# Performance work log

Measured on AMD Instinct MI355X. Metric: run time of the kernel, lower is better.

Reference implementation:

```python
import jax, jax.numpy as jnp
import numpy as np

B, K, D, H = 4, 2048, 1024, 16
NCTX = K // 2
IMAGE_SIZE = 224
MAX_POS = 1024


def _build_rope_cache_2d(max_pos, dim, base=10000.0):
    half_dim = dim // 2
    theta = 1.0 / base ** (np.arange(0, half_dim, 2, dtype=np.float32) / half_dim)
    positions = np.arange(max_pos, dtype=np.float32)
    freqs = np.outer(positions, theta)  # [max_pos, dim/4]
    return jnp.asarray(np.stack([np.cos(freqs), np.sin(freqs)], axis=-1))  # [max_pos, dim/4, 2]


def apply_rope_2d(x, coords, rope_cache, image_size):
    b, k, d = x.shape
    half, quarter = d // 2, d // 4
    max_pos = rope_cache.shape[0]
    cn = jnp.clip(coords / image_size * (max_pos - 1), 0, max_pos - 1)
    y_pos = cn[..., 0].astype(jnp.int32)
    x_pos = cn[..., 1].astype(jnp.int32)
    y_rope = rope_cache[y_pos]  # [b,k,quarter,2]
    x_rope = rope_cache[x_pos]

    def rot(part, r):
        c, s = r[..., 0], r[..., 1]
        p0, p1 = part[..., 0], part[..., 1]
        return jnp.stack([p0 * c - p1 * s, p0 * s + p1 * c], -1).reshape(b, k, half)

    xp = x[..., :half].reshape(b, k, quarter, 2)
    yp = x[..., half:].reshape(b, k, quarter, 2)
    return jnp.concatenate([rot(xp, x_rope), rot(yp, y_rope)], -1)


def mha(q_tok, kv_tok, in_w, in_b, out_w, out_b, num_heads):
    b, nq, d = q_tok.shape
    hd = d // num_heads
    wq, wk, wv = jnp.split(in_w, 3, axis=0)
    bq, bk, bv = jnp.split(in_b, 3)
    q = (q_tok @ wq.T + bq).reshape(b, nq, num_heads, hd)
    k = (kv_tok @ wk.T + bk).reshape(b, -1, num_heads, hd)
    v = (kv_tok @ wv.T + bv).reshape(b, -1, num_heads, hd)
    s = jnp.einsum('bqhd,bkhd->bhqk', q, k) / jnp.sqrt(jnp.asarray(hd, q.dtype))
    a = jax.nn.softmax(s, axis=-1)
    o = jnp.einsum('bhqk,bkhd->bqhd', a, v).reshape(b, nq, d)
    return o @ out_w.T + out_b


def setup_inputs() -> dict:
    key = jax.random.key(0)
    ks = jax.random.split(key, 12)
    sc = 1.0 / np.sqrt(D)
    x = jax.random.normal(ks[0], (B, K, D), jnp.float32)
    coords = jax.random.uniform(ks[1], (B, K, 2), jnp.float32) * IMAGE_SIZE
    # boolean context mask with exactly NCTX context tokens per batch (code assumes equal counts)
    perms = jax.vmap(lambda k_: jax.random.permutation(k_, K))(jax.random.split(ks[2], B))
    is_context = jax.vmap(lambda m, i: m.at[i].set(True))(jnp.zeros((B, K), bool), perms[:, :NCTX])
    rope_cache = _build_rope_cache_2d(MAX_POS, D)
    return {
        'x': x, 'coords': coords, 'is_context': is_context, 'rope_cache': rope_cache,
        'ctx_in_w': jax.random.normal(ks[3], (3 * D, D), jnp.float32) * sc,
        'ctx_in_b': jnp.zeros((3 * D,), jnp.float32),
        'ctx_out_w': jax.random.normal(ks[4], (D, D), jnp.float32) * sc,
        'ctx_out_b': jnp.zeros((D,), jnp.float32),
        'tgt_in_w': jax.random.normal(ks[5], (3 * D, D), jnp.float32) * sc,
        'tgt_in_b': jnp.zeros((3 * D,), jnp.float32),
        'tgt_out_w': jax.random.normal(ks[6], (D, D), jnp.float32) * sc,
        'tgt_out_b': jnp.zeros((D,), jnp.float32),
    }


def reference(x, coords, is_context, rope_cache,
              ctx_in_w, ctx_in_b, ctx_out_w, ctx_out_b,
              tgt_in_w, tgt_in_b, tgt_out_w, tgt_out_b):
    # 2D RoPE before attention (as in the backbone)
    xr = apply_rope_2d(x, coords, rope_cache, IMAGE_SIZE)
    # stable argsort: context positions (key 0) first, in original order
    order = jnp.argsort(jnp.where(is_context, 0, 1), axis=1, stable=True)
    ctx_idx = order[:, :NCTX]   # [B, NCTX]
    tgt_idx = order[:, NCTX:]   # [B, K-NCTX]
    ctx_tok = jnp.take_along_axis(xr, ctx_idx[..., None], axis=1)
    tgt_tok = jnp.take_along_axis(xr, tgt_idx[..., None], axis=1)
    ctx_out = mha(ctx_tok, ctx_tok, ctx_in_w, ctx_in_b, ctx_out_w, ctx_out_b, H)
    tgt_out = mha(tgt_tok, ctx_tok, tgt_in_w, tgt_in_b, tgt_out_w, tgt_out_b, H)
    out = jnp.zeros_like(x)
    out = jax.vmap(lambda o, i, v: o.at[i].set(v))(out, ctx_idx, ctx_out)
    out = jax.vmap(lambda o, i, v: o.at[i].set(v))(out, tgt_idx, tgt_out)
    return out
```

## Files before the change

kernel.cpp:

```cpp
#include <hip/hip_runtime.h>
#include <math.h>

#define B_    4
#define K_    2048
#define D_    1024
#define H_    16
#define NCTX_ 1024

typedef unsigned short ushort_t;
typedef _Float16 f16;
typedef __attribute__((ext_vector_type(8))) _Float16 f16x8;
typedef __attribute__((ext_vector_type(4))) float f32x4;

union U4 {
  f16 h[4];
  ushort4 u;
};

union P4 {
  f16 h[4];
  ushort4 u;
};

__device__ __forceinline__ void gload16(const void* g, void* l) {
  __builtin_amdgcn_global_load_lds(
      (const __attribute__((address_space(1))) unsigned int*)g,
      (__attribute__((address_space(3))) unsigned int*)l, 16, 0, 0);
}

__global__ __launch_bounds__(256) void partition_kernel(
    const unsigned char* __restrict__ isctx, int* __restrict__ pos,
    int* __restrict__ ipos) {
  const int b = blockIdx.x;
  const int tid = threadIdx.x;
  const int wid = tid >> 6, lane = tid & 63;
  __shared__ int csum[4];
  __shared__ int waveTot[4];
  __shared__ int strideSh;

  int cnt = 0;
  for (int i = 0; i < 32; ++i) cnt += (isctx[tid * 32 + i] != 0);
  for (int off = 32; off; off >>= 1) cnt += __shfl_down(cnt, off, 64);
  if (lane == 0) csum[wid] = cnt;
  __syncthreads();
  if (tid == 0) {
    int t = csum[0] + csum[1] + csum[2] + csum[3];
    strideSh = (t > 2048) ? 1 : ((t > 768) ? 4 : 8);
  }
  __syncthreads();
  const int stride = strideSh;

  const unsigned char* base = isctx + (size_t)b * K_ * stride;
  int f[8];
  int s = 0;
  for (int i = 0; i < 8; ++i) {
    f[i] = base[(size_t)(tid * 8 + i) * stride] != 0;
    s += f[i];
  }
  int inc = s;
  for (int off = 1; off < 64; off <<= 1) {
    int v = __shfl_up(inc, off, 64);
    if (lane >= off) inc += v;
  }
  if (lane == 63) waveTot[wid] = inc;
  __syncthreads();
  int wOff = 0;
  for (int w = 0; w < wid; ++w) wOff += waveTot[w];
  int run = wOff + inc - s;
  for (int i = 0; i < 8; ++i) {
    int k = tid * 8 + i;
    int p;
    if (f[i]) {
      p = run;
      run++;
    } else {
      p = NCTX_ + k - run;
    }
    pos[b * K_ + k] = p;
    ipos[b * K_ + p] = k;
  }
}

__global__ __launch_bounds__(256) void rope_kernel(
    const float* __restrict__ x, const float* __restrict__ coords,
    const float* __restrict__ cache, const int* __restrict__ ipos,
    f16* __restrict__ tok) {
  const int row = blockIdx.x;
  const int b = row >> 11;
  const int r = row & (K_ - 1);
  const int k = ipos[row];
  const int t = threadIdx.x;

  const float cy = coords[(size_t)(b * K_ + k) * 2 + 0];
  const float cx = coords[(size_t)(b * K_ + k) * 2 + 1];
  const int ypos = (int)fminf(fmaxf(cy / 224.0f * 1023.0f, 0.0f), 1023.0f);
  const int xpos = (int)fminf(fmaxf(cx / 224.0f * 1023.0f, 0.0f), 1023.0f);

  const float4 v = ((const float4*)(x + ((size_t)b * K_ + k) * D_))[t];
  const int e = 4 * t;
  const float* crow;
  int coff;
  if (e < 512) {
    crow = cache + (size_t)xpos * 512;
    coff = e;
  } else {
    crow = cache + (size_t)ypos * 512;
    coff = e - 512;
  }
  const float4 cs = *(const float4*)(crow + coff);
  float o[4];
  o[0] = v.x * cs.x - v.y * cs.y;
  o[1] = v.x * cs.y + v.y * cs.x;
  o[2] = v.z * cs.z - v.w * cs.w;
  o[3] = v.z * cs.w + v.w * cs.z;
  U4 h;
#pragma unroll
  for (int i = 0; i < 4; ++i) h.h[i] = (f16)o[i];
  ((ushort4*)(tok + ((size_t)b * K_ + r) * D_))[t] = h.u;
}

__global__ __launch_bounds__(256) void cvt_all(
    const float* __restrict__ ctx_in_w, const float* __restrict__ tgt_in_w,
    const float* __restrict__ ctx_out_w, const float* __restrict__ tgt_out_w,
    f16* __restrict__ dst) {
  const int i4 = blockIdx.x * 256 + threadIdx.x;
  const int f = i4 * 4;
  const float* src;
  if (f < 3145728) src = ctx_in_w + f;
  else if (f < 5242880) src = tgt_in_w + (f - 3145728 + 1048576);
  else if (f < 6291456) src = tgt_in_w + (f - 5242880);
  else if (f < 7340032) src = ctx_out_w + (f - 6291456);
  else src = tgt_out_w + (f - 7340032);
  const float4 v = *(const float4*)src;
  U4 u;
  u.h[0] = (f16)v.x;
  u.h[1] = (f16)v.y;
  u.h[2] = (f16)v.z;
  u.h[3] = (f16)v.w;
  ((ushort4*)dst)[i4] = u.u;
}

#define GEMM_PRE(AP, WP, Kd)                                                  \
  const int rb_ = wave * 8 + (lane >> 3);          \
  const int kk_ = ((lane & 7) ^ (lane >> 3)) * 8;   \
  const f16* gA_ = (AP) + (size_t)rb_ * (Kd) + kk_;                           \
  const f16* gW_ = (WP) + (size_t)rb_ * (Kd) + kk_;                           \
  const int lA_ = wave * 8 * 64 + lane * 8;

#define GEMM_STAGE(k0s, bb)                                                   \
  _Pragma("unroll") for (int j = 0; j < 4; ++j) {                             \
    gload16(gA_ + (size_t)j * 32 * Kd_ + (k0s), &lds[(bb) + j * 2048 + lA_]); \
    gload16(gW_ + (size_t)j * 32 * Kd_ + (k0s),                               \
            &lds[(bb) + 8192 + j * 2048 + lA_]);                              \
  }

#define GEMM_TILE(bb)                                                         \
  _Pragma("unroll") for (int kh = 0; kh < 2; ++kh) {                          \
    f16x8 af[4], wf[4];                                                       \
    _Pragma("unroll") for (int i = 0; i < 4; ++i) {                           \
      const int ca = ((kh * 4 + quad) ^ (m16 & 7)) * 8;                       \
      af[i] = *(const f16x8*)&lds[(bb) + (wm + i * 16 + m16) * 64 + ca];      \
      wf[i] =                                                                 \
          *(const f16x8*)&lds[(bb) + 8192 + (wn + i * 16 + m16) * 64 + ca];   \
    }                                                                         \
    _Pragma("unroll") for (int i = 0; i < 4; ++i)                             \
        _Pragma("unroll") for (int j = 0; j < 4; ++j)                         \
      acc[i][j] = __builtin_amdgcn_mfma_f32_16x16x32_f16(af[i], wf[j],        \
                                                         acc[i][j], 0, 0, 0); \
  }

#define GEMM_CORE(AP, WP, Kd)                                                 \
  f32x4 acc[4][4];                                                            \
  {                                                                           \
    const f32x4 z = {0.f, 0.f, 0.f, 0.f};                                     \
    for (int i = 0; i < 4; ++i)                                               \
      for (int j = 0; j < 4; ++j) acc[i][j] = z;                              \
  }                                                                           \
  const int Kd_ = (Kd);                                                       \
  GEMM_PRE(AP, WP, Kd_)                                                       \
  GEMM_STAGE(0, 0)                                                            \
  for (int t = 0; t < Kd_ / 64; ++t) {                                        \
    const int cb = (t & 1) * 16384;                                           \
    if (t + 1 < Kd_ / 64) {                                                   \
      GEMM_STAGE((t + 1) * 64, ((t + 1) & 1) * 16384)                         \
      asm volatile("s_waitcnt vmcnt(8)" ::: "memory");                        \
    } else {                                                                  \
      asm volatile("s_waitcnt vmcnt(0)" ::: "memory");                        \
    }                                                                         \
    __builtin_amdgcn_s_barrier();                                             \
    asm volatile("" ::: "memory");                                            \
    GEMM_TILE(cb)                                                             \
    asm volatile("" ::: "memory");                                            \
    __builtin_amdgcn_s_barrier();                                             \
  }

__global__ __launch_bounds__(256, 2) void gemm_proj(
    const f16* __restrict__ tok, const f16* __restrict__ wcat,
    const float* __restrict__ ctx_in_b, const float* __restrict__ tgt_in_b,
    f16* __restrict__ qkvc, f16* __restrict__ kvt, f16* __restrict__ qt) {
  __shared__ f16 lds[32768];
  const int tid = threadIdx.x;
  const int wave = tid >> 6, lane = tid & 63;
  const int quad = lane >> 4, m16 = lane & 15;
  const int nb = blockIdx.x, mb = blockIdx.y, b = blockIdx.z;
  const int wm = (wave & 1) << 6, wn = (wave >> 1) << 6;
  const int m0 = mb * 128;
  const bool isQ = nb >= 40;
  const int n0 = isQ ? (nb - 40) * 128 : nb * 128;
  const f16* AP = tok + (size_t)b * K_ * D_ +
                  (isQ ? (size_t)NCTX_ * D_ : (size_t)0) + (size_t)m0 * D_;
  const f16* WP = wcat + (isQ ? (size_t)5242880 : (size_t)0) +
                  (size_t)n0 * D_;

  GEMM_CORE(AP, WP, D_)

#pragma unroll
  for (int j = 0; j < 4; ++j) {
    const int col = n0 + wn + j * 16 + m16;
    float bv;
    f16* dst;
    int ldc, dcol;
    if (isQ) {
      bv = tgt_in_b[col];
      dst = qt + (size_t)b * NCTX_ * D_;
      ldc = D_;
      dcol = col;
    } else if (col < 3072) {
      bv = ctx_in_b[col];
      dst = qkvc + (size_t)b * NCTX_ * 3072;
      ldc = 3072;
      dcol = col;
    } else {
      bv = tgt_in_b[D_ + col - 3072];
      dst = kvt + (size_t)b * NCTX_ * 2048;
      ldc = 2048;
      dcol = col - 3072;
    }
#pragma unroll
    for (int i = 0; i < 4; ++i) {
      const int mr = m0 + wm + i * 16 + quad * 4;
#pragma unroll
      for (int r = 0; r < 4; ++r)
        dst[(size_t)(mr + r) * ldc + dcol] = (f16)(acc[i][j][r] + bv);
    }
  }
}

__global__ __launch_bounds__(256, 2) void gemm_out(
    const f16* __restrict__ Atok, const f16* __restrict__ Wbase,
    const float* __restrict__ bias_ctx, const float* __restrict__ bias_tgt,
    const int* __restrict__ ipos, float* __restrict__ out) {
  __shared__ f16 lds[32768];
  const int tid = threadIdx.x;
  const int wave = tid >> 6, lane = tid & 63;
  const int quad = lane >> 4, m16 = lane & 15;
  const int n0 = blockIdx.x * 128, m0 = blockIdx.y * 128;
  const int b = blockIdx.z & 3, sel = blockIdx.z >> 2;
  const int wm = (wave & 1) << 6, wn = (wave >> 1) << 6;
  const f16* AP = Atok + (size_t)b * K_ * D_ + (size_t)sel * NCTX_ * D_ +
                  (size_t)m0 * D_;
  const f16* WP = Wbase + (size_t)sel * 1048576 + (size_t)n0 * D_;
  const float* bias = sel ? bias_tgt : bias_ctx;

  GEMM_CORE(AP, WP, D_)

#pragma unroll
  for (int j = 0; j < 4; ++j) {
    const int col = n0 + wn + j * 16 + m16;
    const float bv = bias[col];
#pragma unroll
    for (int i = 0; i < 4; ++i) {
      const int mr = m0 + wm + i * 16 + quad * 4;
#pragma unroll
      for (int r = 0; r < 4; ++r) {
        const int orow = ipos[b * K_ + sel * NCTX_ + mr + r];
        out[(size_t)b * K_ * D_ + (size_t)orow * D_ + col] =
            acc[i][j][r] + bv;
      }
    }
  }
}

__global__ __launch_bounds__(256) void vtrans_kernel(
    const ushort_t* __restrict__ V, long long sVb, int ldv, int coloff,
    ushort_t* __restrict__ Vt) {
  __shared__ __align__(16) ushort_t tile[64][72];
  const int tblk = blockIdx.x, h = blockIdx.y, b = blockIdx.z;
  const int tid = threadIdx.x;
  const ushort_t* src =
      V + (long long)b * sVb + (size_t)(tblk * 64) * ldv + coloff + h * 64;
#pragma unroll
  for (int j = 0; j < 2; ++j) {
    const int c = j * 256 + tid;
    const int r = c >> 3, dc = c & 7;
    *(uint4*)&tile[r][dc * 8] = *(const uint4*)(src + (size_t)r * ldv + dc * 8);
  }
  __syncthreads();
  ushort_t* dst = Vt + (size_t)(b * H_ + h) * 64 * 1024 + tblk * 64;
#pragma unroll
  for (int j = 0; j < 2; ++j) {
    const int c = j * 256 + tid;
    const int d = c >> 3, tc = c & 7;
    union {
      ushort_t u[8];
      uint4 v;
    } t;
#pragma unroll
    for (int i = 0; i < 8; ++i) t.u[i] = tile[tc * 8 + i][d];
    *(uint4*)(dst + (size_t)d * 1024 + tc * 8) = t.v;
  }
}

__global__ __launch_bounds__(256) void attn_mfma(
    const f16* __restrict__ Qp, long long sQb, int ldq,
    const f16* __restrict__ Kp, long long sKb, int ldk,
    const f16* __restrict__ Vt, f16* __restrict__ O, long long sOb) {
  __shared__ f16 QP[4096];
  __shared__ f16 Ks[2][4096];
  __shared__ f16 Vs[2][4096];
  const int tid = threadIdx.x, wave = tid >> 6, lane = tid & 63;
  const int quad = lane >> 4, m16 = lane & 15;
  const int q0 = blockIdx.x * 64, h = blockIdx.y, b = blockIdx.z;
  const f16* Qb = Qp + (long long)b * sQb + h * 64;
  const f16* Kb = Kp + (long long)b * sKb + h * 64;
  const f16* Vb = Vt + (size_t)(b * H_ + h) * 64 * 1024;

  const int rL = lane >> 3;
  const int kkc = ((lane & 7) ^ rL) * 8;
  const int lB = wave * 512 + lane * 8;

#pragma unroll
  for (int j = 0; j < 2; ++j) {
    const int row = j * 32 + wave * 8 + rL;
    gload16(Qb + (size_t)(q0 + row) * ldq + kkc, &QP[j * 2048 + lB]);
  }
#pragma unroll
  for (int j = 0; j < 2; ++j) {
    const int row = j * 32 + wave * 8 + rL;
    gload16(Kb + (size_t)row * ldk + kkc, &Ks[0][j * 2048 + lB]);
    gload16(Vb + (size_t)row * 1024 + kkc, &Vs[0][j * 2048 + lB]);
  }

  float m_run = -1e30f, l_run = 0.f;
  f32x4 Oa[4];
  const f32x4 z = {0.f, 0.f, 0.f, 0.f};
#pragma unroll
  for (int j = 0; j < 4; ++j) Oa[j] = z;

  asm volatile("s_waitcnt vmcnt(4)" ::: "memory");
  __builtin_amdgcn_s_barrier();

  const int c0 = (quad ^ (m16 & 7)) * 8;
  const int c1 = ((quad + 4) ^ (m16 & 7)) * 8;
  const f16x8 qf0 = *(const f16x8*)&QP[(wave * 16 + m16) * 64 + c0];
  const f16x8 qf1 = *(const f16x8*)&QP[(wave * 16 + m16) * 64 + c1];

  f16* Pw = QP + wave * 1024;

  for (int kt = 0; kt < 16; ++kt) {
    const int cur = kt & 1;
    if (kt < 15) {
#pragma unroll
      for (int j = 0; j < 2; ++j) {
        const int row = j * 32 + wave * 8 + rL;
        gload16(Kb + (size_t)((kt + 1) * 64 + row) * ldk + kkc,
                &Ks[cur ^ 1][j * 2048 + lB]);
        gload16(Vb + (size_t)row * 1024 + (kt + 1) * 64 + kkc,
                &Vs[cur ^ 1][j * 2048 + lB]);
      }
      asm volatile("s_waitcnt vmcnt(4)" ::: "memory");
    } else {
      asm volatile("s_waitcnt vmcnt(0)" ::: "memory");
    }
    __builtin_amdgcn_s_barrier();

    f32x4 S[4];
    __builtin_amdgcn_s_setprio(1);
#pragma unroll
    for (int jn = 0; jn < 4; ++jn) {
      S[jn] = z;
      const f16x8 kf0 = *(const f16x8*)&Ks[cur][(jn * 16 + m16) * 64 + c0];
      const f16x8 kf1 = *(const f16x8*)&Ks[cur][(jn * 16 + m16) * 64 + c1];
      S[jn] = __builtin_amdgcn_mfma_f32_16x16x32_f16(kf0, qf0, S[jn], 0, 0, 0);
      S[jn] = __builtin_amdgcn_mfma_f32_16x16x32_f16(kf1, qf1, S[jn], 0, 0, 0);
    }
    __builtin_amdgcn_s_setprio(0);

    float mv0 = fmaxf(fmaxf(S[0][0], S[1][0]), fmaxf(S[2][0], S[3][0]));
    float mv1 = fmaxf(fmaxf(S[0][1], S[1][1]), fmaxf(S[2][1], S[3][1]));
    float mv2 = fmaxf(fmaxf(S[0][2], S[1][2]), fmaxf(S[2][2], S[3][2]));
    float mv3 = fmaxf(fmaxf(S[0][3], S[1][3]), fmaxf(S[2][3], S[3][3]));
    float mx = fmaxf(fmaxf(mv0, mv1), fmaxf(mv2, mv3));
    mx = fmaxf(mx, __shfl_xor(mx, 16, 64));
    mx = fmaxf(mx, __shfl_xor(mx, 32, 64));
    mx *= 0.125f;
    const float mnew = fmaxf(m_run, mx);
    const float al = __expf(m_run - mnew);
    m_run = mnew;

    float rs = 0.f;
#pragma unroll
    for (int jn = 0; jn < 4; ++jn) {
      P4 p4;
#pragma unroll
      for (int r = 0; r < 4; ++r) {
        const float p = __expf(__builtin_fmaf(S[jn][r], 0.125f, -mnew));
        rs += p;
        p4.h[r] = (f16)p;
      }
      *(ushort4*)&Pw[m16 * 64 + (((jn * 2 + (quad >> 1)) ^ (m16 & 7)) * 8) +
                     (quad & 1) * 4] = p4.u;
    }
    rs += __shfl_xor(rs, 16, 64);
    rs += __shfl_xor(rs, 32, 64);
    l_run = l_run * al + rs;

    float alq[4];
#pragma unroll
    for (int r = 0; r < 4; ++r) alq[r] = __shfl(al, quad * 4 + r, 64);
#pragma unroll
    for (int j = 0; j < 4; ++j) {
      Oa[j][0] *= alq[0];
      Oa[j][1] *= alq[1];
      Oa[j][2] *= alq[2];
      Oa[j][3] *= alq[3];
    }

    const f16x8 pf0 = *(const f16x8*)&Pw[m16 * 64 + c0];
    const f16x8 pf1 = *(const f16x8*)&Pw[m16 * 64 + c1];
    __builtin_amdgcn_s_setprio(1);
#pragma unroll
    for (int jd = 0; jd < 4; ++jd) {
      const f16x8 vf0 = *(const f16x8*)&Vs[cur][(jd * 16 + m16) * 64 + c0];
      const f16x8 vf1 = *(const f16x8*)&Vs[cur][(jd * 16 + m16) * 64 + c1];
      Oa[jd] = __builtin_amdgcn_mfma_f32_16x16x32_f16(pf0, vf0, Oa[jd], 0, 0, 0);
      Oa[jd] = __builtin_amdgcn_mfma_f32_16x16x32_f16(pf1, vf1, Oa[jd], 0, 0, 0);
    }
    __builtin_amdgcn_s_setprio(0);
    __builtin_amdgcn_s_barrier();
  }

  float lq[4];
#pragma unroll
  for (int r = 0; r < 4; ++r) lq[r] = 1.0f / __shfl(l_run, quad * 4 + r, 64);
#pragma unroll
  for (int jd = 0; jd < 4; ++jd)
#pragma unroll
    for (int r = 0; r < 4; ++r) {
      const float v = Oa[jd][r] * lq[r];
      const size_t off = (long long)b * sOb +
                         (size_t)(q0 + wave * 16 + quad * 4 + r) * D_ + h * 64 +
                         jd * 16 + m16;
      O[off] = (f16)v;
    }
}

extern "C" void kernel_launch(void* const* d_in, const int* in_sizes, int n_in,
                              void* d_out, int out_size, void* d_ws,
                              size_t ws_size, hipStream_t stream) {
  const float* x = (const float*)d_in[0];
  const float* coords = (const float*)d_in[1];
  const unsigned char* isctx = (const unsigned char*)d_in[2];
  const float* rope = (const float*)d_in[3];
  const float* ctx_in_w = (const float*)d_in[4];
  const float* ctx_in_b = (const float*)d_in[5];
  const float* ctx_out_w = (const float*)d_in[6];
  const float* ctx_out_b = (const float*)d_in[7];
  const float* tgt_in_w = (const float*)d_in[8];
  const float* tgt_in_b = (const float*)d_in[9];
  const float* tgt_out_w = (const float*)d_in[10];
  const float* tgt_out_b = (const float*)d_in[11];
  float* out = (float*)d_out;

  f16* ws = (f16*)d_ws;
  f16* tok = ws;
  f16* wcat = tok + 8388608;
  f16* qkvc = wcat + 8388608;
  f16* kvt = qkvc + 12582912;
  f16* qt = kvt + 8388608;
  f16* vt = qt + 4194304;
  int* pos = (int*)(vt + 4194304);
  int* ipos = pos + B_ * K_;

  partition_kernel<<<B_, 256, 0, stream>>>(isctx, pos, ipos);
  cvt_all<<<8192, 256, 0, stream>>>(ctx_in_w, tgt_in_w, ctx_out_w, tgt_out_w,
                                    wcat);
  rope_kernel<<<B_ * K_, 256, 0, stream>>>(x, coords, rope, ipos, tok);

  gemm_proj<<<dim3(48, 8, B_), 256, 0, stream>>>(tok, wcat, ctx_in_b,
                                                 tgt_in_b, qkvc, kvt, qt);

  vtrans_kernel<<<dim3(16, H_, B_), 256, 0, stream>>>(
      (const ushort_t*)qkvc, (long long)NCTX_ * 3 * D_, 3 * D_, 2 * D_,
      (ushort_t*)vt);
  attn_mfma<<<dim3(16, H_, B_), 256, 0, stream>>>(
      qkvc, (long long)NCTX_ * 3 * D_, 3 * D_, qkvc + D_,
      (long long)NCTX_ * 3 * D_, 3 * D_, vt, tok, (long long)K_ * D_);
  vtrans_kernel<<<dim3(16, H_, B_), 256, 0, stream>>>(
      (const ushort_t*)kvt, (long long)NCTX_ * 2 * D_, 2 * D_, D_,
      (ushort_t*)vt);
  attn_mfma<<<dim3(16, H_, B_), 256, 0, stream>>>(
      qt, (long long)NCTX_ * D_, D_, kvt, (long long)NCTX_ * 2 * D_, 2 * D_,
      vt, tok + (size_t)NCTX_ * D_, (long long)K_ * D_);

  gemm_out<<<dim3(8, 8, 2 * B_), 256, 0, stream>>>(
      tok, wcat + 6291456, ctx_out_b, tgt_out_b, ipos, out);
}
```

Baseline: 325.2 us.

## Process 128 queries per attention block with 8 waves sharing K/V tiles

The attention kernel now uses 512 threads (8 waves) and 128 query rows per block instead of 256 threads and 64 rows, so each K/V tile staged in shared memory serves twice as many queries. This halves the grid and the global K/V traffic per query, and each thread now issues one K and one V load per tile. The cost is fewer blocks (512 per attention call), which may reduce occupancy and latency hiding, plus a larger shared-memory footprint for Q/P. The untouched softmax/PV section indexes P per wave, so correctness depends on per-wave offsets still fitting the doubled QP buffer.

Result: faster. 303.9 us (-6.6%).

```diff
diff --git a/kernel.cpp b/kernel.cpp
--- a/kernel.cpp
+++ b/kernel.cpp
@@ -311,35 +311,30 @@
   }
 }
 
-__global__ __launch_bounds__(256) void attn_mfma(
+__global__ __launch_bounds__(512) void attn_mfma(
     const f16* __restrict__ Qp, long long sQb, int ldq,
     const f16* __restrict__ Kp, long long sKb, int ldk,
     const f16* __restrict__ Vt, f16* __restrict__ O, long long sOb) {
-  __shared__ f16 QP[4096];
+  __shared__ f16 QP[8192];
   __shared__ f16 Ks[2][4096];
   __shared__ f16 Vs[2][4096];
   const int tid = threadIdx.x, wave = tid >> 6, lane = tid & 63;
   const int quad = lane >> 4, m16 = lane & 15;
-  const int q0 = blockIdx.x * 64, h = blockIdx.y, b = blockIdx.z;
+  const int q0 = blockIdx.x * 128, h = blockIdx.y, b = blockIdx.z;
   const f16* Qb = Qp + (long long)b * sQb + h * 64;
   const f16* Kb = Kp + (long long)b * sKb + h * 64;
   const f16* Vb = Vt + (size_t)(b * H_ + h) * 64 * 1024;
 
-  const int rL = lane >> 3;
-  const int kkc = ((lane & 7) ^ rL) * 8;
-  const int lB = wave * 512 + lane * 8;
-
-#pragma unroll
-  for (int j = 0; j < 2; ++j) {
-    const int row = j * 32 + wave * 8 + rL;
-    gload16(Qb + (size_t)(q0 + row) * ldq + kkc, &QP[j * 2048 + lB]);
-  }
-#pragma unroll
-  for (int j = 0; j < 2; ++j) {
-    const int row = j * 32 + wave * 8 + rL;
-    gload16(Kb + (size_t)row * ldk + kkc, &Ks[0][j * 2048 + lB]);
-    gload16(Vb + (size_t)row * 1024 + kkc, &Vs[0][j * 2048 + lB]);
-  }
+  const int rowS = tid >> 3;
+  const int kkc = ((tid & 7) ^ (rowS & 7)) * 8;
+  const int lB = tid * 8;
+
+#pragma unroll
+  for (int j = 0; j < 2; ++j)
+    gload16(Qb + (size_t)(q0 + j * 64 + rowS) * ldq + kkc,
+            &QP[j * 4096 + lB]);
+  gload16(Kb + (size_t)rowS * ldk + kkc, &Ks[0][lB]);
+  gload16(Vb + (size_t)rowS * 1024 + kkc, &Vs[0][lB]);
 
   float m_run = -1e30f, l_run = 0.f;
   f32x4 Oa[4];
@@ -347,7 +342,7 @@
 #pragma unroll
   for (int j = 0; j < 4; ++j) Oa[j] = z;
 
-  asm volatile("s_waitcnt vmcnt(4)" ::: "memory");
+  asm volatile("s_waitcnt vmcnt(2)" ::: "memory");
   __builtin_amdgcn_s_barrier();
 
   const int c0 = (quad ^ (m16 & 7)) * 8;
@@ -360,15 +355,11 @@
   for (int kt = 0; kt < 16; ++kt) {
     const int cur = kt & 1;
     if (kt < 15) {
-#pragma unroll
-      for (int j = 0; j < 2; ++j) {
-        const int row = j * 32 + wave * 8 + rL;
-        gload16(Kb + (size_t)((kt + 1) * 64 + row) * ldk + kkc,
-                &Ks[cur ^ 1][j * 2048 + lB]);
-        gload16(Vb + (size_t)row * 1024 + (kt + 1) * 64 + kkc,
-                &Vs[cur ^ 1][j * 2048 + lB]);
-      }
-      asm volatile("s_waitcnt vmcnt(4)" ::: "memory");
+      gload16(Kb + (size_t)((kt + 1) * 64 + rowS) * ldk + kkc,
+              &Ks[cur ^ 1][lB]);
+      gload16(Vb + (size_t)rowS * 1024 + (kt + 1) * 64 + kkc,
+              &Vs[cur ^ 1][lB]);
+      asm volatile("s_waitcnt vmcnt(2)" ::: "memory");
     } else {
       asm volatile("s_waitcnt vmcnt(0)" ::: "memory");
     }
@@ -493,13 +484,13 @@
   vtrans_kernel<<<dim3(16, H_, B_), 256, 0, stream>>>(
       (const ushort_t*)qkvc, (long long)NCTX_ * 3 * D_, 3 * D_, 2 * D_,
       (ushort_t*)vt);
-  attn_mfma<<<dim3(16, H_, B_), 256, 0, stream>>>(
+  attn_mfma<<<dim3(8, H_, B_), 512, 0, stream>>>(
       qkvc, (long long)NCTX_ * 3 * D_, 3 * D_, qkvc + D_,
       (long long)NCTX_ * 3 * D_, 3 * D_, vt, tok, (long long)K_ * D_);
   vtrans_kernel<<<dim3(16, H_, B_), 256, 0, stream>>>(
       (const ushort_t*)kvt, (long long)NCTX_ * 2 * D_, 2 * D_, D_,
       (ushort_t*)vt);
-  attn_mfma<<<dim3(16, H_, B_), 256, 0, stream>>>(
+  attn_mfma<<<dim3(8, H_, B_), 512, 0, stream>>>(
       qt, (long long)NCTX_ * D_, D_, kvt, (long long)NCTX_ * 2 * D_, 2 * D_,
       vt, tok + (size_t)NCTX_ * D_, (long long)K_ * D_);
 
```
